# Kernel optimization log

Measured on AMD Instinct MI355X. Metric: run time of the kernel, lower is better.

## Reference

```python
import jax, jax.numpy as jnp
import numpy as np

H, D = 8, 16            # heads, per-head dim (hidden_channels // heads)
HID = H * D             # 128
N_MAT, N_ELEM = 100000, 118
F_MAT, F_ELEM = 128, 64
OUT = 64
E_EM, E_MM = 1000000, 2000000
NEG_SLOPE = 0.2

def _k(i):
    return jax.random.fold_in(jax.random.key(0), i)

def setup_inputs() -> dict:
    p = lambda i, shape: 0.1 * jax.random.normal(_k(i), shape, dtype=jnp.float32)
    return dict(
        x_mat=jax.random.normal(_k(0), (N_MAT, F_MAT), dtype=jnp.float32),
        x_elem=jax.random.normal(_k(1), (N_ELEM, F_ELEM), dtype=jnp.float32),
        W_proj_mat=p(2, (HID, F_MAT)), b_proj_mat=p(3, (HID,)),
        W_proj_elem=p(4, (HID, F_ELEM)), b_proj_elem=p(5, (HID,)),
        a_src_em=p(6, (H, D)), a_dst_em=p(7, (H, D)),
        a_src_mm=p(8, (H, D)), a_dst_mm=p(9, (H, D)),
        Wk=p(10, (HID, HID)), bk=p(11, (HID,)), q=p(12, (HID,)),
        Wl=p(13, (OUT, HID)), bl=p(14, (OUT,)),
        src_em=jax.random.randint(_k(15), (E_EM,), 0, N_ELEM, dtype=jnp.int32),
        dst_em=jax.random.randint(_k(16), (E_EM,), 0, N_MAT, dtype=jnp.int32),
        src_mm=jax.random.randint(_k(17), (E_MM,), 0, N_MAT, dtype=jnp.int32),
        dst_mm=jax.random.randint(_k(18), (E_MM,), 0, N_MAT, dtype=jnp.int32),
    )

def _edge_type_conv(x_s, x_d, a_s, a_d, src, dst, n_dst):
    # x_s:[Ns,H,D], x_d:[Nd,H,D]; per-edge-type GAT-style attention (HANConv.message)
    alpha = jnp.sum(x_s * a_s, -1)[src] + jnp.sum(x_d * a_d, -1)[dst]   # [E,H]
    alpha = jax.nn.leaky_relu(alpha, NEG_SLOPE)
    amax = jax.ops.segment_max(alpha, dst, num_segments=n_dst)          # stable softmax per dst
    ex = jnp.exp(alpha - amax[dst])
    den = jax.ops.segment_sum(ex, dst, num_segments=n_dst)
    w = ex / (den[dst] + 1e-16)                                         # [E,H]
    out = jax.ops.segment_sum(x_s[src] * w[:, :, None], dst, num_segments=n_dst)  # [Nd,H,D]
    return jax.nn.relu(out.reshape(n_dst, HID))

def _group(xs, q, Wk, bk):
    # HANConv semantic-level attention over metapaths
    s = jnp.stack(xs)                                                   # [M,N,C]
    score = jnp.sum(q * jnp.mean(jnp.tanh(s @ Wk.T + bk), axis=1), axis=-1)  # [M]
    attn = jax.nn.softmax(score)
    return jnp.einsum('m,mnc->nc', attn, s)

def reference(x_mat, x_elem, W_proj_mat, b_proj_mat, W_proj_elem, b_proj_elem,
              a_src_em, a_dst_em, a_src_mm, a_dst_mm, Wk, bk, q, Wl, bl,
              src_em, dst_em, src_mm, dst_mm):
    h_mat = (x_mat @ W_proj_mat.T + b_proj_mat).reshape(N_MAT, H, D)
    h_elem = (x_elem @ W_proj_elem.T + b_proj_elem).reshape(N_ELEM, H, D)
    o_em = _edge_type_conv(h_elem, h_mat, a_src_em, a_dst_em, src_em, dst_em, N_MAT)
    o_mm = _edge_type_conv(h_mat, h_mat, a_src_mm, a_dst_mm, src_mm, dst_mm, N_MAT)
    out_mat = _group([o_em, o_mm], q, Wk, bk)                           # [N_MAT, HID]
    return out_mat @ Wl.T + bl                                          # final Linear
```

## Files before the change

kernel.cpp:

```cpp
#include <hip/hip_runtime.h>
#include <hip/hip_bf16.h>

typedef unsigned int uint32;
typedef unsigned short ushort16;

using bf16x8 = __attribute__((ext_vector_type(8))) short;
using f32x4  = __attribute__((ext_vector_type(4))) float;

#define N_MATN 100000
#define N_ELEMN 118
#define F_MATN 128
#define F_ELEMN 64
#define HIDN 128
#define NHEAD 8
#define OUTC 64
#define NSTRIPS 6250
#define NT2 16
#define NTILES2 (N_MATN/NT2)

#define MATBLK 1024
#define CNTBLK 128

#define SH 8
#define NBK 391
#define BCH 8192

__device__ __forceinline__ float blo(uint32 u){ return __uint_as_float(u << 16); }
__device__ __forceinline__ float bhi(uint32 u){ return __uint_as_float(u & 0xffff0000u); }
__device__ __forceinline__ ushort16 f2bf(float f){
    uint32 u = __float_as_uint(f);
    uint32 r = u + 0x7FFFu + ((u >> 16) & 1u);
    return (ushort16)(r >> 16);
}
__device__ __forceinline__ uint32 pack2(float a, float b){
    return (uint32)f2bf(a) | ((uint32)f2bf(b) << 16);
}
__device__ __forceinline__ bf16x8 cvt8(const float* __restrict__ p){
    bf16x8 r;
    #pragma unroll
    for(int j=0;j<8;j++) r[j] = (short)f2bf(p[j]);
    return r;
}

__global__ __launch_bounds__(256) void proj_all(
    const float* __restrict__ xe, const float* __restrict__ We,
    const float* __restrict__ be, const float* __restrict__ a_se,
    ushort16* __restrict__ h_elem, float* __restrict__ asrc_em,
    const float* __restrict__ x, const float* __restrict__ W,
    const float* __restrict__ bias,
    const float* __restrict__ a_de, const float* __restrict__ a_sm, const float* __restrict__ a_dm,
    ushort16* __restrict__ h,
    float* __restrict__ adst_em, float* __restrict__ asrc_mm, float* __restrict__ adst_mm,
    const int* __restrict__ dst_em, int nE_em, int* __restrict__ bcnt_em,
    const int* __restrict__ dst_mm, int nE_mm, int* __restrict__ bcnt_mm)
{
    int tid = threadIdx.x;
    if(blockIdx.x < N_ELEMN){
        __shared__ float xr[F_ELEMN];
        int n = blockIdx.x, c = tid;
        if(c < 16) ((float4*)xr)[c] = ((const float4*)(xe + n*F_ELEMN))[c];
        __syncthreads();
        if(c < 128){
            const float4* Wr = (const float4*)(We + c*F_ELEMN);
            float acc = 0.f;
            #pragma unroll 4
            for(int i=0;i<16;i++){
                float4 w = Wr[i];
                acc += xr[4*i]*w.x + xr[4*i+1]*w.y + xr[4*i+2]*w.z + xr[4*i+3]*w.w;
            }
            acc += be[c];
            h_elem[n*HIDN + c] = f2bf(acc);
            float p = acc * a_se[c];
            #pragma unroll
            for(int m=8;m>=1;m>>=1) p += __shfl_xor(p, m, 16);
            if((c&15)==0) asrc_em[n*NHEAD + (c>>4)] = p;
        }
        return;
    }
    if(blockIdx.x >= N_ELEMN + MATBLK){
        __shared__ int he[NBK], hm[NBK];
        for(int i=tid;i<NBK;i+=256){ he[i]=0; hm[i]=0; }
        __syncthreads();
        int cb = blockIdx.x - (N_ELEMN + MATBLK);
        int gt = cb*256 + tid;
        int st = CNTBLK*256;
        {
            int n4 = nE_em >> 2;
            const int4* d4 = (const int4*)dst_em;
            for(int i = gt; i < n4; i += st){
                int4 v = d4[i];
                atomicAdd(&he[v.x>>SH],1); atomicAdd(&he[v.y>>SH],1);
                atomicAdd(&he[v.z>>SH],1); atomicAdd(&he[v.w>>SH],1);
            }
            for(int i = (n4<<2) + gt; i < nE_em; i += st) atomicAdd(&he[dst_em[i]>>SH],1);
        }
        {
            int n4 = nE_mm >> 2;
            const int4* d4 = (const int4*)dst_mm;
            for(int i = gt; i < n4; i += st){
                int4 v = d4[i];
                atomicAdd(&hm[v.x>>SH],1); atomicAdd(&hm[v.y>>SH],1);
                atomicAdd(&hm[v.z>>SH],1); atomicAdd(&hm[v.w>>SH],1);
            }
            for(int i = (n4<<2) + gt; i < nE_mm; i += st) atomicAdd(&hm[dst_mm[i]>>SH],1);
        }
        __syncthreads();
        for(int j=tid;j<NBK;j+=256){
            int a = he[j], b = hm[j];
            if(a) atomicAdd(&bcnt_em[j], a);
            if(b) atomicAdd(&bcnt_mm[j], b);
        }
        return;
    }
    int wv = tid >> 6, lane = tid & 63, quad = lane >> 4, sl = lane & 15;
    bf16x8 B[2][4];
    float bc[2], ade[2], asv[2], adv[2];
    #pragma unroll
    for(int i=0;i<2;i++){
        int c = (2*wv+i)*16 + sl;
        const float* wr = W + c*F_MATN;
        #pragma unroll
        for(int ks=0;ks<4;ks++) B[i][ks] = cvt8(wr + ks*32 + quad*8);
        bc[i] = bias[c]; ade[i] = a_de[c]; asv[i] = a_sm[c]; adv[i] = a_dm[c];
    }
    for(int s = blockIdx.x - N_ELEMN; s < NSTRIPS; s += MATBLK){
        int n0 = s*16;
        const float* xrow = x + (size_t)(n0+sl)*F_MATN;
        bf16x8 A[4];
        #pragma unroll
        for(int ks=0;ks<4;ks++) A[ks] = cvt8(xrow + ks*32 + quad*8);
        f32x4 acc[2];
        #pragma unroll
        for(int i=0;i<2;i++){ acc[i][0]=0.f; acc[i][1]=0.f; acc[i][2]=0.f; acc[i][3]=0.f; }
        #pragma unroll
        for(int i=0;i<2;i++)
            #pragma unroll
            for(int ks=0;ks<4;ks++)
                acc[i] = __builtin_amdgcn_mfma_f32_16x16x32_bf16(A[ks], B[i][ks], acc[i], 0, 0, 0);
        #pragma unroll
        for(int i=0;i<2;i++){
            int head = 2*wv + i;
            #pragma unroll
            for(int r=0;r<4;r++){
                float a = acc[i][r] + bc[i];
                int node = n0 + quad*4 + r;
                h[(size_t)node*HIDN + head*16 + sl] = f2bf(a);
                float p0 = a*ade[i], p1 = a*asv[i], p2 = a*adv[i];
                #pragma unroll
                for(int m=8;m>=1;m>>=1){
                    p0 += __shfl_xor(p0, m);
                    p1 += __shfl_xor(p1, m);
                    p2 += __shfl_xor(p2, m);
                }
                if(sl == 0){
                    adst_em[node*NHEAD + head] = p0;
                    asrc_mm[node*NHEAD + head] = p1;
                    adst_mm[node*NHEAD + head] = p2;
                }
            }
        }
    }
}

__global__ __launch_bounds__(512) void bucket_scan(
    const int* __restrict__ bcnt_em, int* __restrict__ bb_em, int* __restrict__ bcur_em,
    const int* __restrict__ bcnt_mm, int* __restrict__ bb_mm, int* __restrict__ bcur_mm,
    int* __restrict__ offs_em, int* __restrict__ offs_mm, int nE_em, int nE_mm)
{
    __shared__ int wsum[8];
    int t = threadIdx.x, l = t & 63, w = t >> 6;
    {
        int v = (t < NBK) ? bcnt_em[t] : 0;
        int x = v;
        #pragma unroll
        for(int off=1; off<64; off<<=1){ int y = __shfl_up(x, off); if(l >= off) x += y; }
        if(l == 63) wsum[w] = x;
        __syncthreads();
        int base = 0;
        for(int k=0;k<w;k++) base += wsum[k];
        int excl = base + x - v;
        if(t < NBK){ bb_em[t] = excl; bcur_em[t] = excl; }
        if(t == 0){ bb_em[NBK] = nE_em; offs_em[N_MATN] = nE_em; }
        __syncthreads();
    }
    {
        int v = (t < NBK) ? bcnt_mm[t] : 0;
        int x = v;
        #pragma unroll
        for(int off=1; off<64; off<<=1){ int y = __shfl_up(x, off); if(l >= off) x += y; }
        if(l == 63) wsum[w] = x;
        __syncthreads();
        int base = 0;
        for(int k=0;k<w;k++) base += wsum[k];
        int excl = base + x - v;
        if(t < NBK){ bb_mm[t] = excl; bcur_mm[t] = excl; }
        if(t == 0){ bb_mm[NBK] = nE_mm; offs_mm[N_MATN] = nE_mm; }
    }
}

__global__ __launch_bounds__(256) void bin_pass(
    const int* __restrict__ src_em, const int* __restrict__ dst_em, int nE_em,
    int* __restrict__ bcur_em, uint32* __restrict__ st_em,
    const int* __restrict__ src_mm, const int* __restrict__ dst_mm, int nE_mm,
    int* __restrict__ bcur_mm, uint32* __restrict__ st_mm)
{
    __shared__ int cnt[NBK];
    __shared__ int base[NBK];
    int t = threadIdx.x;
    int nch_em = (nE_em + BCH - 1)/BCH;
    int nch_mm = (nE_mm + BCH - 1)/BCH;
    int ntot = nch_em + nch_mm;
    for(int c = blockIdx.x; c < ntot; c += gridDim.x){
        bool em = c < nch_em;
        const int* src = em ? src_em : src_mm;
        const int* dst = em ? dst_em : dst_mm;
        int nE   = em ? nE_em : nE_mm;
        int* bcur = em ? bcur_em : bcur_mm;
        uint32* st = em ? st_em : st_mm;
        int cc = em ? c : c - nch_em;
        int s = cc*BCH;
        int e = s + BCH; if(e > nE) e = nE;
        int len = e - s;
        int n4 = len >> 2;
        const int4* d4 = (const int4*)(dst + s);
        const int4* s4 = (const int4*)(src + s);
        for(int i=t;i<NBK;i+=256) cnt[i] = 0;
        __syncthreads();
        for(int i=t;i<n4;i+=256){
            int4 v = d4[i];
            atomicAdd(&cnt[v.x>>SH],1); atomicAdd(&cnt[v.y>>SH],1);
            atomicAdd(&cnt[v.z>>SH],1); atomicAdd(&cnt[v.w>>SH],1);
        }
        for(int i = s + (n4<<2) + t; i < e; i += 256) atomicAdd(&cnt[dst[i]>>SH], 1);
        __syncthreads();
        for(int i=t;i<NBK;i+=256){
            int v = cnt[i];
            base[i] = v ? atomicAdd(&bcur[i], v) : 0;
            cnt[i] = 0;
        }
        __syncthreads();
        for(int i=t;i<n4;i+=256){
            int4 dv = d4[i];
            int4 sv = s4[i];
            int b, p;
            b = dv.x>>SH; p = base[b] + atomicAdd(&cnt[b],1);
            st[p] = ((uint32)(dv.x & ((1<<SH)-1)) << 17) | (uint32)sv.x;
            b = dv.y>>SH; p = base[b] + atomicAdd(&cnt[b],1);
            st[p] = ((uint32)(dv.y & ((1<<SH)-1)) << 17) | (uint32)sv.y;
            b = dv.z>>SH; p = base[b] + atomicAdd(&cnt[b],1);
            st[p] = ((uint32)(dv.z & ((1<<SH)-1)) << 17) | (uint32)sv.z;
            b = dv.w>>SH; p = base[b] + atomicAdd(&cnt[b],1);
            st[p] = ((uint32)(dv.w & ((1<<SH)-1)) << 17) | (uint32)sv.w;
        }
        for(int i = s + (n4<<2) + t; i < e; i += 256){
            int d = dst[i];
            int b = d >> SH;
            int p = base[b] + atomicAdd(&cnt[b], 1);
            st[p] = ((uint32)(d & ((1<<SH)-1)) << 17) | (uint32)src[i];
        }
        __syncthreads();
    }
}

__global__ __launch_bounds__(256) void place_pass(
    const int* __restrict__ bb_em, const uint32* __restrict__ st_em,
    int* __restrict__ csr_em, int* __restrict__ offs_em,
    const int* __restrict__ bb_mm, const uint32* __restrict__ st_mm,
    int* __restrict__ csr_mm, int* __restrict__ offs_mm)
{
    __shared__ int cnt[256];
    __shared__ int wsum[4];
    __shared__ int cur[256];
    int b = blockIdx.x;
    bool em = b < NBK;
    const int* bb        = em ? bb_em : bb_mm;
    const uint32* stp    = em ? st_em : st_mm;
    int* csr             = em ? csr_em : csr_mm;
    int* offs            = em ? offs_em : offs_mm;
    int bk = em ? b : b - NBK;
    int d0 = bk << SH;
    int t = threadIdx.x, l = t & 63, w = t >> 6;
    int nd = N_MATN - d0; if(nd > 256) nd = 256;
    int beg = bb[bk], end = bb[bk+1];
    cnt[t] = 0;
    __syncthreads();
    for(int i = beg + t; i < end; i += 256)
        atomicAdd(&cnt[stp[i] >> 17], 1);
    __syncthreads();
    int v = cnt[t];
    int x = v;
    #pragma unroll
    for(int off=1; off<64; off<<=1){ int y = __shfl_up(x, off); if(l >= off) x += y; }
    if(l == 63) wsum[w] = x;
    __syncthreads();
    int base = beg;
    for(int k=0;k<w;k++) base += wsum[k];
    int excl = base + x - v;
    cur[t] = excl;
    if(t < nd) offs[d0 + t] = excl;
    __syncthreads();
    for(int i = beg + t; i < end; i += 256){
        uint32 vv = stp[i];
        int dl = (int)(vv >> 17);
        int p = atomicAdd(&cur[dl], 1);
        csr[p] = (int)(vv & 0x1FFFFu);
    }
}

__global__ __launch_bounds__(256) void agg_both(
    const int* __restrict__ offs_em, const int* __restrict__ csr_em,
    const ushort16* __restrict__ h_elem, const float* __restrict__ asrc_em,
    const float* __restrict__ adst_em, ushort16* __restrict__ o_em,
    const int* __restrict__ offs_mm, const int* __restrict__ csr_mm,
    const ushort16* __restrict__ h_mat, const float* __restrict__ asrc_mm,
    const float* __restrict__ adst_mm, ushort16* __restrict__ o_mm)
{
    int lane = threadIdx.x & 63;
    int g = lane >> 4;
    int q = lane & 15;
    int hd = q >> 1;
    int w = (blockIdx.x*blockDim.x + threadIdx.x) >> 6;
    int nw = (gridDim.x*blockDim.x) >> 6;
    for(int nid = w; nid < 2*N_MATN; nid += nw){
        int nidu = __builtin_amdgcn_readfirstlane(nid);
        bool em = nidu < N_MATN;
        int d = em ? nidu : nidu - N_MATN;
        const int*    offs = em ? offs_em : offs_mm;
        const int*    csr  = em ? csr_em  : csr_mm;
        const uint32* hs   = (const uint32*)(em ? h_elem : h_mat);
        const float*  asp  = em ? asrc_em : asrc_mm;
        const float*  adp  = em ? adst_em : adst_mm;
        uint32*       op   = (uint32*)(em ? o_em : o_mm);
        int beg = offs[d], end = offs[d+1];
        float ad = adp[(unsigned)(d*NHEAD + hd)];
        float denA = 0.f, denB = 0.f;
        float nloA[4] = {0.f,0.f,0.f,0.f}, nhiA[4] = {0.f,0.f,0.f,0.f};
        float nloB[4] = {0.f,0.f,0.f,0.f}, nhiB[4] = {0.f,0.f,0.f,0.f};
        for(int j0 = beg; j0 < end; j0 += 8){
            int e0 = j0 + g, e1 = j0 + 4 + g;
            bool v0 = e0 < end, v1 = e1 < end;
            int s0 = csr[(unsigned)(v0 ? e0 : end - 1)];
            int s1 = csr[(unsigned)(v1 ? e1 : end - 1)];
            float a0 = asp[(unsigned)(s0*NHEAD + hd)];
            float a1 = asp[(unsigned)(s1*NHEAD + hd)];
            const uint4 h0 = *(const uint4*)(hs + (unsigned)(s0*64 + q*4));
            const uint4 h1 = *(const uint4*)(hs + (unsigned)(s1*64 + q*4));
            float al0 = a0 + ad; al0 = fmaxf(al0, 0.2f*al0);
            float ex0 = __expf(al0); ex0 = v0 ? ex0 : 0.f;
            float al1 = a1 + ad; al1 = fmaxf(al1, 0.2f*al1);
            float ex1 = __expf(al1); ex1 = v1 ? ex1 : 0.f;
            denA += ex0; denB += ex1;
            nloA[0] += blo(h0.x)*ex0; nhiA[0] += bhi(h0.x)*ex0;
            nloA[1] += blo(h0.y)*ex0; nhiA[1] += bhi(h0.y)*ex0;
            nloA[2] += blo(h0.z)*ex0; nhiA[2] += bhi(h0.z)*ex0;
            nloA[3] += blo(h0.w)*ex0; nhiA[3] += bhi(h0.w)*ex0;
            nloB[0] += blo(h1.x)*ex1; nhiB[0] += bhi(h1.x)*ex1;
            nloB[1] += blo(h1.y)*ex1; nhiB[1] += bhi(h1.y)*ex1;
            nloB[2] += blo(h1.z)*ex1; nhiB[2] += bhi(h1.z)*ex1;
            nloB[3] += blo(h1.w)*ex1; nhiB[3] += bhi(h1.w)*ex1;
        }
        float den = denA + denB;
        den += __shfl_xor(den, 16); den += __shfl_xor(den, 32);
        float nlo[4], nhi[4];
        #pragma unroll
        for(int k=0;k<4;k++){
            nlo[k] = nloA[k] + nloB[k];
            nhi[k] = nhiA[k] + nhiB[k];
            nlo[k] += __shfl_xor(nlo[k], 16); nlo[k] += __shfl_xor(nlo[k], 32);
            nhi[k] += __shfl_xor(nhi[k], 16); nhi[k] += __shfl_xor(nhi[k], 32);
        }
        if(g == 0){
            float rdn = 1.0f/(den + 1e-16f);
            uint4 pk;
            pk.x = pack2(fmaxf(nlo[0]*rdn, 0.f), fmaxf(nhi[0]*rdn, 0.f));
            pk.y = pack2(fmaxf(nlo[1]*rdn, 0.f), fmaxf(nhi[1]*rdn, 0.f));
            pk.z = pack2(fmaxf(nlo[2]*rdn, 0.f), fmaxf(nhi[2]*rdn, 0.f));
            pk.w = pack2(fmaxf(nlo[3]*rdn, 0.f), fmaxf(nhi[3]*rdn, 0.f));
            *(uint4*)(op + (size_t)d*64 + q*4) = pk;
        }
    }
}

__global__ __launch_bounds__(256) void score_mfma(
    const ushort16* __restrict__ o_em, const ushort16* __restrict__ o_mm,
    const float* __restrict__ Wk, const float* __restrict__ bkv,
    const float* __restrict__ qv, float* __restrict__ scores)
{
    int tid = threadIdx.x;
    int wv = tid >> 6, lane = tid & 63, quad = lane >> 4, sl = lane & 15;
    bf16x8 B[2][4];
    float bkc[2], qc[2];
    #pragma unroll
    for(int i=0;i<2;i++){
        int c = (2*wv+i)*16 + sl;
        const float* wr = Wk + c*HIDN;
        #pragma unroll
        for(int ks=0;ks<4;ks++) B[i][ks] = cvt8(wr + ks*32 + quad*8);
        bkc[i] = bkv[c]; qc[i] = qv[c];
    }
    float se = 0.f, sm = 0.f;
    for(int s = blockIdx.x; s < NSTRIPS; s += gridDim.x){
        int n0 = s*16;
        const bf16x8* rowE = (const bf16x8*)(o_em + (size_t)(n0+sl)*HIDN);
        const bf16x8* rowM = (const bf16x8*)(o_mm + (size_t)(n0+sl)*HIDN);
        bf16x8 AE[4], AM[4];
        #pragma unroll
        for(int ks=0;ks<4;ks++){
            AE[ks] = rowE[ks*4 + quad];
            AM[ks] = rowM[ks*4 + quad];
        }
        f32x4 aE[2], aM[2];
        #pragma unroll
        for(int i=0;i<2;i++){
            aE[i][0]=0.f;aE[i][1]=0.f;aE[i][2]=0.f;aE[i][3]=0.f;
            aM[i][0]=0.f;aM[i][1]=0.f;aM[i][2]=0.f;aM[i][3]=0.f;
        }
        #pragma unroll
        for(int i=0;i<2;i++)
            #pragma unroll
            for(int ks=0;ks<4;ks++){
                aE[i] = __builtin_amdgcn_mfma_f32_16x16x32_bf16(AE[ks], B[i][ks], aE[i], 0, 0, 0);
                aM[i] = __builtin_amdgcn_mfma_f32_16x16x32_bf16(AM[ks], B[i][ks], aM[i], 0, 0, 0);
            }
        #pragma unroll
        for(int i=0;i<2;i++)
            #pragma unroll
            for(int r=0;r<4;r++){
                se += qc[i]*tanhf(aE[i][r] + bkc[i]);
                sm += qc[i]*tanhf(aM[i][r] + bkc[i]);
            }
    }
    #pragma unroll
    for(int m=32;m>=1;m>>=1){ se += __shfl_xor(se,m); sm += __shfl_xor(sm,m); }
    __shared__ float red[8];
    if(lane==0){ red[wv*2]=se; red[wv*2+1]=sm; }
    __syncthreads();
    if(tid==0){
        atomicAdd(&scores[0], red[0]+red[2]+red[4]+red[6]);
        atomicAdd(&scores[1], red[1]+red[3]+red[5]+red[7]);
    }
}

__global__ __launch_bounds__(256) void final_v4(
    const ushort16* __restrict__ o_em, const ushort16* __restrict__ o_mm,
    const float* __restrict__ Wl, const float* __restrict__ blv,
    const float* __restrict__ scores, float* __restrict__ out)
{
    __shared__ float wlds[64*129];
    __shared__ float zlds[NT2*128];
    int t = threadIdx.x;
    for(int i=t;i<2048;i+=256){
        float4 v = ((const float4*)Wl)[i];
        int r = i >> 5, k4 = i & 31;
        float* d = wlds + r*129 + k4*4;
        d[0]=v.x; d[1]=v.y; d[2]=v.z; d[3]=v.w;
    }
    float s0 = scores[0]*(1.0f/N_MATN), s1 = scores[1]*(1.0f/N_MATN);
    float mx = fmaxf(s0,s1);
    float e0 = __expf(s0-mx), e1 = __expf(s1-mx);
    float inv = 1.0f/(e0+e1);
    float a0 = e0*inv, a1 = e1*inv;
    int j = t & 63, half = t >> 6;
    float bj = blv[j];
    const float* wr = wlds + j*129;
    __syncthreads();
    for(int tile = blockIdx.x; tile < NTILES2; tile += gridDim.x){
        int n0 = tile*NT2;
        __syncthreads();
        {
            const uint4* pe = (const uint4*)((const uint32*)o_em + (size_t)n0*64);
            const uint4* pm = (const uint4*)((const uint32*)o_mm + (size_t)n0*64);
            uint4 ve = pe[t], vm = pm[t];
            float* zd = zlds + t*8;
            zd[0]=a0*blo(ve.x)+a1*blo(vm.x); zd[1]=a0*bhi(ve.x)+a1*bhi(vm.x);
            zd[2]=a0*blo(ve.y)+a1*blo(vm.y); zd[3]=a0*bhi(ve.y)+a1*bhi(vm.y);
            zd[4]=a0*blo(ve.z)+a1*blo(vm.z); zd[5]=a0*bhi(ve.z)+a1*bhi(vm.z);
            zd[6]=a0*blo(ve.w)+a1*blo(vm.w); zd[7]=a0*bhi(ve.w)+a1*bhi(vm.w);
        }
        __syncthreads();
        float acc[4] = {0.f,0.f,0.f,0.f};
        #pragma unroll 1
        for(int kk=0;kk<128;kk+=8){
            float f0=wr[kk],f1=wr[kk+1],f2=wr[kk+2],f3=wr[kk+3];
            float f4=wr[kk+4],f5=wr[kk+5],f6=wr[kk+6],f7=wr[kk+7];
            #pragma unroll
            for(int n=0;n<4;n++){
                const float4* zr = (const float4*)(zlds + (half*4+n)*128 + kk);
                float4 za = zr[0], zb = zr[1];
                acc[n] += za.x*f0 + za.y*f1 + za.z*f2 + za.w*f3
                        + zb.x*f4 + zb.y*f5 + zb.z*f6 + zb.w*f7;
            }
        }
        #pragma unroll
        for(int n=0;n<4;n++)
            out[(size_t)(n0 + half*4 + n)*OUTC + j] = bj + acc[n];
    }
}

extern "C" void kernel_launch(void* const* d_in, const int* in_sizes, int n_in,
                              void* d_out, int out_size, void* d_ws, size_t ws_size,
                              hipStream_t stream)
{
    const float* x_mat    = (const float*)d_in[0];
    const float* x_elem   = (const float*)d_in[1];
    const float* W_pm     = (const float*)d_in[2];
    const float* b_pm     = (const float*)d_in[3];
    const float* W_pe     = (const float*)d_in[4];
    const float* b_pe     = (const float*)d_in[5];
    const float* a_se     = (const float*)d_in[6];
    const float* a_de     = (const float*)d_in[7];
    const float* a_sm     = (const float*)d_in[8];
    const float* a_dm     = (const float*)d_in[9];
    const float* Wk       = (const float*)d_in[10];
    const float* bk       = (const float*)d_in[11];
    const float* qv       = (const float*)d_in[12];
    const float* Wl       = (const float*)d_in[13];
    const float* bl       = (const float*)d_in[14];
    const int* src_em     = (const int*)d_in[15];
    const int* dst_em     = (const int*)d_in[16];
    const int* src_mm     = (const int*)d_in[17];
    const int* dst_mm     = (const int*)d_in[18];
    int nE_em = in_sizes[15];
    int nE_mm = in_sizes[17];

    char* ws = (char*)d_ws;
    size_t off = 0;
    auto alloc = [&](size_t bytes) -> void* {
        void* p = ws + off; off += (bytes + 255) & ~size_t(255); return p;
    };
    ushort16* h_mat   = (ushort16*)alloc((size_t)N_MATN*HIDN*2);
    ushort16* h_elem  = (ushort16*)alloc((size_t)N_ELEMN*HIDN*2);
    float*    asrcEM  = (float*)   alloc((size_t)N_ELEMN*NHEAD*4);
    float*    adstEM  = (float*)   alloc((size_t)N_MATN*NHEAD*4);
    float*    asrcMM  = (float*)   alloc((size_t)N_MATN*NHEAD*4);
    float*    adstMM  = (float*)   alloc((size_t)N_MATN*NHEAD*4);
    int*      offs_em = (int*)     alloc((size_t)(N_MATN+1)*4);
    int*      offs_mm = (int*)     alloc((size_t)(N_MATN+1)*4);
    int*      csr_em  = (int*)     alloc((size_t)1000000*4);
    int*      csr_mm  = (int*)     alloc((size_t)2000000*4);
    ushort16* o_em    = (ushort16*)alloc((size_t)N_MATN*HIDN*2);
    ushort16* o_mm    = (ushort16*)alloc((size_t)N_MATN*HIDN*2);
    int*      bb_em   = (int*)     alloc((size_t)(NBK+1)*4);
    int*      bb_mm   = (int*)     alloc((size_t)(NBK+1)*4);
    int*      bcur_em = (int*)     alloc((size_t)NBK*4);
    int*      bcur_mm = (int*)     alloc((size_t)NBK*4);
    size_t zero_start = off;
    int*      bcnt_em = (int*)     alloc((size_t)NBK*4);
    int*      bcnt_mm = (int*)     alloc((size_t)NBK*4);
    float*    scores  = (float*)   alloc(256);
    size_t zero_bytes = off - zero_start;

    uint32* st_em = (uint32*)o_em;
    uint32* st_mm = st_em + nE_em;

    hipMemsetAsync(ws + zero_start, 0, zero_bytes, stream);

    proj_all<<<N_ELEMN + MATBLK + CNTBLK, 256, 0, stream>>>(
        x_elem, W_pe, b_pe, a_se, h_elem, asrcEM,
        x_mat, W_pm, b_pm, a_de, a_sm, a_dm,
        h_mat, adstEM, asrcMM, adstMM,
        dst_em, nE_em, bcnt_em, dst_mm, nE_mm, bcnt_mm);

    bucket_scan<<<1, 512, 0, stream>>>(bcnt_em, bb_em, bcur_em,
                                       bcnt_mm, bb_mm, bcur_mm,
                                       offs_em, offs_mm, nE_em, nE_mm);

    int nch = (nE_em + BCH - 1)/BCH + (nE_mm + BCH - 1)/BCH;
    bin_pass<<<nch, 256, 0, stream>>>(src_em, dst_em, nE_em, bcur_em, st_em,
                                      src_mm, dst_mm, nE_mm, bcur_mm, st_mm);
    place_pass<<<2*NBK, 256, 0, stream>>>(bb_em, st_em, csr_em, offs_em,
                                          bb_mm, st_mm, csr_mm, offs_mm);

    agg_both<<<4096, 256, 0, stream>>>(offs_em, csr_em, h_elem, asrcEM, adstEM, o_em,
                                       offs_mm, csr_mm, h_mat, asrcMM, adstMM, o_mm);

    score_mfma<<<1024, 256, 0, stream>>>(o_em, o_mm, Wk, bk, qv, scores);
    final_v4<<<2048, 256, 0, stream>>>(o_em, o_mm, Wl, bl, scores, (float*)d_out);
}
```

Measured before the change: 468.3 us.

## Use bf16 MFMA for the final linear layer instead of scalar LDS GEMM

Rewrites the final projection kernel so each wavefront processes a 16-row strip with 16x16x32 bf16 MFMA instructions. Wl is held in registers as bf16 fragments and the LDS staging and block barriers are removed. The attention-weighted combination of the two metapath outputs is computed in registers and rounded to bf16 before the matrix multiply. This cuts FP32 ALU and LDS traffic in the final GEMM, at the cost of extra bf16 rounding error on the combined activations and the weights.

```diff
diff --git a/kernel.cpp b/kernel.cpp
--- a/kernel.cpp
+++ b/kernel.cpp
@@ -15,8 +15,6 @@
 #define NHEAD 8
 #define OUTC 64
 #define NSTRIPS 6250
-#define NT2 16
-#define NTILES2 (N_MATN/NT2)
 
 #define MATBLK 1024
 #define CNTBLK 128
@@ -441,59 +439,63 @@
     }
 }
 
-__global__ __launch_bounds__(256) void final_v4(
+__global__ __launch_bounds__(256) void final_mfma(
     const ushort16* __restrict__ o_em, const ushort16* __restrict__ o_mm,
     const float* __restrict__ Wl, const float* __restrict__ blv,
     const float* __restrict__ scores, float* __restrict__ out)
 {
-    __shared__ float wlds[64*129];
-    __shared__ float zlds[NT2*128];
-    int t = threadIdx.x;
-    for(int i=t;i<2048;i+=256){
-        float4 v = ((const float4*)Wl)[i];
-        int r = i >> 5, k4 = i & 31;
-        float* d = wlds + r*129 + k4*4;
-        d[0]=v.x; d[1]=v.y; d[2]=v.z; d[3]=v.w;
+    int tid = threadIdx.x;
+    int lane = tid & 63, quad = lane >> 4, sl = lane & 15;
+    bf16x8 B[4][4];
+    float blc[4];
+    #pragma unroll
+    for(int i=0;i<4;i++){
+        int c = i*16 + sl;
+        const float* wr = Wl + c*HIDN;
+        #pragma unroll
+        for(int ks=0;ks<4;ks++) B[i][ks] = cvt8(wr + ks*32 + quad*8);
+        blc[i] = blv[c];
     }
     float s0 = scores[0]*(1.0f/N_MATN), s1 = scores[1]*(1.0f/N_MATN);
     float mx = fmaxf(s0,s1);
     float e0 = __expf(s0-mx), e1 = __expf(s1-mx);
     float inv = 1.0f/(e0+e1);
     float a0 = e0*inv, a1 = e1*inv;
-    int j = t & 63, half = t >> 6;
-    float bj = blv[j];
-    const float* wr = wlds + j*129;
-    __syncthreads();
-    for(int tile = blockIdx.x; tile < NTILES2; tile += gridDim.x){
-        int n0 = tile*NT2;
-        __syncthreads();
-        {
-            const uint4* pe = (const uint4*)((const uint32*)o_em + (size_t)n0*64);
-            const uint4* pm = (const uint4*)((const uint32*)o_mm + (size_t)n0*64);
-            uint4 ve = pe[t], vm = pm[t];
-            float* zd = zlds + t*8;
-            zd[0]=a0*blo(ve.x)+a1*blo(vm.x); zd[1]=a0*bhi(ve.x)+a1*bhi(vm.x);
-            zd[2]=a0*blo(ve.y)+a1*blo(vm.y); zd[3]=a0*bhi(ve.y)+a1*bhi(vm.y);
-            zd[4]=a0*blo(ve.z)+a1*blo(vm.z); zd[5]=a0*bhi(ve.z)+a1*bhi(vm.z);
-            zd[6]=a0*blo(ve.w)+a1*blo(vm.w); zd[7]=a0*bhi(ve.w)+a1*bhi(vm.w);
-        }
-        __syncthreads();
-        float acc[4] = {0.f,0.f,0.f,0.f};
-        #pragma unroll 1
-        for(int kk=0;kk<128;kk+=8){
-            float f0=wr[kk],f1=wr[kk+1],f2=wr[kk+2],f3=wr[kk+3];
-            float f4=wr[kk+4],f5=wr[kk+5],f6=wr[kk+6],f7=wr[kk+7];
-            #pragma unroll
-            for(int n=0;n<4;n++){
-                const float4* zr = (const float4*)(zlds + (half*4+n)*128 + kk);
-                float4 za = zr[0], zb = zr[1];
-                acc[n] += za.x*f0 + za.y*f1 + za.z*f2 + za.w*f3
-                        + zb.x*f4 + zb.y*f5 + zb.z*f6 + zb.w*f7;
-            }
-        }
-        #pragma unroll
-        for(int n=0;n<4;n++)
-            out[(size_t)(n0 + half*4 + n)*OUTC + j] = bj + acc[n];
+    int gw = (blockIdx.x*blockDim.x + tid) >> 6;
+    int nwv = (gridDim.x*blockDim.x) >> 6;
+    for(int s = gw; s < NSTRIPS; s += nwv){
+        int n0 = s*16;
+        const uint4* rowE = (const uint4*)((const uint32*)o_em + (size_t)(n0+sl)*64);
+        const uint4* rowM = (const uint4*)((const uint32*)o_mm + (size_t)(n0+sl)*64);
+        bf16x8 A[4];
+        #pragma unroll
+        for(int ks=0;ks<4;ks++){
+            uint4 e = rowE[ks*4 + quad];
+            uint4 m = rowM[ks*4 + quad];
+            bf16x8 a;
+            a[0] = (short)f2bf(a0*blo(e.x)+a1*blo(m.x));
+            a[1] = (short)f2bf(a0*bhi(e.x)+a1*bhi(m.x));
+            a[2] = (short)f2bf(a0*blo(e.y)+a1*blo(m.y));
+            a[3] = (short)f2bf(a0*bhi(e.y)+a1*bhi(m.y));
+            a[4] = (short)f2bf(a0*blo(e.z)+a1*blo(m.z));
+            a[5] = (short)f2bf(a0*bhi(e.z)+a1*bhi(m.z));
+            a[6] = (short)f2bf(a0*blo(e.w)+a1*blo(m.w));
+            a[7] = (short)f2bf(a0*bhi(e.w)+a1*bhi(m.w));
+            A[ks] = a;
+        }
+        f32x4 acc[4];
+        #pragma unroll
+        for(int i=0;i<4;i++){ acc[i][0]=0.f; acc[i][1]=0.f; acc[i][2]=0.f; acc[i][3]=0.f; }
+        #pragma unroll
+        for(int i=0;i<4;i++)
+            #pragma unroll
+            for(int ks=0;ks<4;ks++)
+                acc[i] = __builtin_amdgcn_mfma_f32_16x16x32_bf16(A[ks], B[i][ks], acc[i], 0, 0, 0);
+        #pragma unroll
+        for(int i=0;i<4;i++)
+            #pragma unroll
+            for(int r=0;r<4;r++)
+                out[(size_t)(n0 + quad*4 + r)*OUTC + i*16 + sl] = acc[i][r] + blc[i];
     }
 }
 
@@ -575,5 +577,5 @@
                                        offs_mm, csr_mm, h_mat, asrcMM, adstMM, o_mm);
 
     score_mfma<<<1024, 256, 0, stream>>>(o_em, o_mm, Wk, bk, qv, scores);
-    final_v4<<<2048, 256, 0, stream>>>(o_em, o_mm, Wl, bl, scores, (float*)d_out);
-}
+    final_mfma<<<1563, 256, 0, stream>>>(o_em, o_mm, Wl, bl, scores, (float*)d_out);
+}
```

Result: faster. 448.1 us (-4.3%).
